# Performance work log

Measured on AMD Instinct MI355X. Metric: run time of the kernel, lower is better.

The kernel has to match this reference:

```python
import jax, jax.numpy as jnp
from jax import lax
import numpy as np

GAMMA = 1.0
BIG = 1e10  # stand-in for +inf; exp(-BIG/gamma) underflows to 0 and keeps grads finite


def pairwise_sq_euclidean(A, B):
    # A: (B,T1,K), B: (B,T2,K) -> (B,T1,T2); 0.5*||a-b||^2 expanded to avoid (B,T1,T2,K)
    aa = 0.5 * jnp.sum(A * A, axis=-1)  # (B,T1)
    bb = 0.5 * jnp.sum(B * B, axis=-1)  # (B,T2)
    ab = jnp.einsum('bik,bjk->bij', A, B)
    return aa[:, :, None] + bb[:, None, :] - ab


def soft_dtw(C, gamma):
    # C: (B, m, n). Sequential DP: V[i,j] = C[i-1,j-1] + softmin_gamma(V[i,j-1], V[i-1,j-1], V[i-1,j])
    Bsz, m, n = C.shape
    dt = C.dtype
    big = jnp.asarray(BIG, dt)
    # row 0 of V: V[0,0]=0, V[0,j]=inf
    v0 = jnp.concatenate([jnp.zeros((Bsz, 1), dt), jnp.full((Bsz, n), big, dt)], axis=1)

    def row_step(v_prev, c_row):
        # v_prev: (B, n+1) = V[i-1, :]; c_row: (B, n) = C[:, i-1, :]
        def col_step(v_left, inp):
            c, v_diag, v_up = inp  # each (B,)
            prev = jnp.stack([v_left, v_diag, v_up], axis=-1)  # (B,3)
            minv = -gamma * jax.nn.logsumexp(-prev / gamma, axis=-1)
            v_new = c + minv
            return v_new, v_new

        xs = (c_row.T, v_prev[:, :-1].T, v_prev[:, 1:].T)  # (n, B) each
        _, vals = lax.scan(col_step, jnp.full((Bsz,), big, dt), xs)
        v_row = jnp.concatenate([jnp.full((Bsz, 1), big, dt), vals.T], axis=1)
        return v_row, None

    v_final, _ = lax.scan(row_step, v0, jnp.moveaxis(C, 1, 0))
    return v_final[:, -1]  # (B,)


def setup_inputs() -> dict:
    key = jax.random.key(0)
    k1, k2 = jax.random.split(key)
    X = jax.random.normal(k1, (512, 256, 64), dtype=jnp.float32)
    Y = jax.random.normal(k2, (512, 256, 64), dtype=jnp.float32)
    return {"X": X, "Y": Y}


def reference(X, Y):
    gamma = jnp.asarray(GAMMA, X.dtype)
    s_xy = soft_dtw(pairwise_sq_euclidean(X, Y), gamma)
    s_xx = soft_dtw(pairwise_sq_euclidean(X, X), gamma)
    s_yy = soft_dtw(pairwise_sq_euclidean(Y, Y), gamma)
    D = s_xy - 0.5 * s_xx - 0.5 * s_yy
    # normalize=False, reduction='mean'
    return jnp.mean(D)
```

## Files before the change

kernel.cpp:

```cpp
#include <hip/hip_runtime.h>

typedef _Float16 h2 __attribute__((ext_vector_type(2)));
typedef _Float16 h8 __attribute__((ext_vector_type(8)));
typedef float f4 __attribute__((ext_vector_type(4)));

#define TT 256
#define KK 64
#define BIGV 1e10f
#define LOG2E 1.44269504f
#define LN2 0.69314718f
#define RL 32
#define RSTR 65

__device__ __forceinline__ float softmin3b(float a, float b, float c) {
  float m, d, M;
  asm("v_min3_f32 %0, %1, %2, %3" : "=v"(m) : "v"(a), "v"(b), "v"(c));
  asm("v_max3_f32 %0, %1, %2, %3" : "=v"(M) : "v"(a), "v"(b), "v"(c));
  asm("v_med3_f32 %0, %1, %2, %3" : "=v"(d) : "v"(a), "v"(b), "v"(c));
  float s = 1.0f + __builtin_amdgcn_exp2f(m - d) + __builtin_amdgcn_exp2f(m - M);
  return m - __log2f(s);
}

__global__ __launch_bounds__(64, 2)
void sdtw_fused1(const float* __restrict__ X, const float* __restrict__ Y,
                 float* __restrict__ out) {
  const int p = blockIdx.x;
  const int type = p >> 9;
  const int b = p & 511;
  const float* Ap = (type == 2 ? Y : X) + (size_t)b * TT * KK;
  const float* Bp = (type == 1 ? X : Y) + (size_t)b * TT * KK;
  const float wgt = (type == 0) ? (LN2 / 512.0f) : (-LN2 / 1024.0f);

  __shared__ unsigned int ring0[RL * RSTR];
  __shared__ unsigned int ring1[RL * RSTR];
  __shared__ float saa[TT];
  __shared__ float sbb[TT];

  const int t = threadIdx.x;
  const int hk = t >> 4, lr = t & 15;

  #pragma unroll
  for (int i = 0; i < 33; ++i) {
    int idx = i * 64 + t;
    if (idx < RL * RSTR) { ring0[idx] = 0u; ring1[idx] = 0u; }
  }

  h8 af[16][2];
  #pragma unroll
  for (int Rt = 0; Rt < 16; ++Rt) {
    float s = 0.f;
    #pragma unroll
    for (int kk = 0; kk < 2; ++kk) {
      const float4* src = (const float4*)(Ap + (Rt * 16 + lr) * KK + kk * 32 + hk * 8);
      float4 x = src[0], y = src[1];
      af[Rt][kk] = (h8){(_Float16)x.x, (_Float16)x.y, (_Float16)x.z, (_Float16)x.w,
                        (_Float16)y.x, (_Float16)y.y, (_Float16)y.z, (_Float16)y.w};
      s += x.x * x.x + x.y * x.y + x.z * x.z + x.w * x.w
         + y.x * y.x + y.y * y.y + y.z * y.z + y.w * y.w;
    }
    s += __shfl_xor(s, 16);
    s += __shfl_xor(s, 32);
    if (hk == (Rt & 3)) saa[Rt * 16 + lr] = 0.5f * LOG2E * s;
  }

  h8 bwin[4][2];
  float vL1 = BIGV, vL2 = BIGV, vL3 = BIGV, vL4 = BIGV;
  float dg = (t == 0) ? 0.0f : BIGV;

  #pragma unroll 1
  for (int kbo = 0; kbo < 5; ++kbo) {
    #pragma unroll
    for (int q = 0; q < 4; ++q) {
      const int KB = kbo * 4 + q;
      if (KB <= 15) {
        float s2 = 0.f;
        #pragma unroll
        for (int kk = 0; kk < 2; ++kk) {
          const float4* src = (const float4*)(Bp + (KB * 16 + lr) * KK + kk * 32 + hk * 8);
          float4 x = src[0], y = src[1];
          bwin[q][kk] = (h8){(_Float16)x.x, (_Float16)x.y, (_Float16)x.z, (_Float16)x.w,
                             (_Float16)y.x, (_Float16)y.y, (_Float16)y.z, (_Float16)y.w};
          s2 += x.x * x.x + x.y * x.y + x.z * x.z + x.w * x.w
              + y.x * y.x + y.y * y.y + y.z * y.z + y.w * y.w;
        }
        s2 += __shfl_xor(s2, 16);
        s2 += __shfl_xor(s2, 32);
        if (hk == 0) sbb[KB * 16 + lr] = 0.5f * LOG2E * s2;
      }
      if (KB <= 18) {
        #pragma unroll
        for (int r = 0; r < 4; ++r) {
          const int k = KB * 4 + r;
          #pragma unroll
          for (int dlt = 0; dlt < 4; ++dlt) {
            if (dlt <= KB && dlt >= KB - 15) {
              const int Rt = r + 4 * dlt;
              const int Ct = KB - dlt;
              const int slot = (q - dlt) & 3;
              f4 acc = {0.f, 0.f, 0.f, 0.f};
              acc = __builtin_amdgcn_mfma_f32_16x16x32_f16(af[Rt][0], bwin[slot][0], acc, 0, 0, 0);
              acc = __builtin_amdgcn_mfma_f32_16x16x32_f16(af[Rt][1], bwin[slot][1], acc, 0, 0, 0);
              const int r0 = Rt * 16 + hk * 4;
              f4 aav = *(const f4*)&saa[r0];
              float bbv = sbb[Ct * 16 + lr];
              float c0 = fmaf(-LOG2E, acc.x, aav.x + bbv);
              float c1 = fmaf(-LOG2E, acc.y, aav.y + bbv);
              float c2 = fmaf(-LOG2E, acc.z, aav.z + bbv);
              float c3 = fmaf(-LOG2E, acc.w, aav.w + bbv);
              const int t_row = 4 * Rt + hk;
              const int s1 = Ct * 16 + lr + t_row;
              const int widx = (s1 & 31) * RSTR + t_row;
              ring0[widx] = __builtin_bit_cast(unsigned int, __builtin_amdgcn_cvt_pkrtz(c0, c1));
              ring1[widx] = __builtin_bit_cast(unsigned int, __builtin_amdgcn_cvt_pkrtz(c2, c3));
            }
          }
          unsigned int w0[4], w1[4];
          #pragma unroll
          for (int u = 0; u < 4; ++u) {
            const int s1 = 4 * k + u;
            const int ridx = (s1 & 31) * RSTR + t;
            w0[u] = ring0[ridx];
            w1[u] = ring1[ridx];
          }
          #pragma unroll
          for (int u = 0; u < 4; ++u) {
            float up1 = __shfl_up(vL4, 1);
            if (t == 0) up1 = BIGV;
            h2 cA = __builtin_bit_cast(h2, w0[u]);
            h2 cB = __builtin_bit_cast(h2, w1[u]);
            float v1 = (float)cA[0] + softmin3b(vL1, dg, up1);
            float v2 = (float)cA[1] + softmin3b(vL2, vL1, v1);
            float v3 = (float)cB[0] + softmin3b(vL3, vL2, v2);
            float v4 = (float)cB[1] + softmin3b(vL4, vL3, v3);
            vL1 = v1; vL2 = v2; vL3 = v3; vL4 = v4; dg = up1;
          }
        }
      }
    }
  }

  #pragma unroll
  for (int u = 0; u < 15; ++u) {
    const int s1 = 304 + u;
    const int ridx = (s1 & 31) * RSTR + t;
    unsigned int a0 = ring0[ridx];
    unsigned int a1 = ring1[ridx];
    float up1 = __shfl_up(vL4, 1);
    if (t == 0) up1 = BIGV;
    h2 cA = __builtin_bit_cast(h2, a0);
    h2 cB = __builtin_bit_cast(h2, a1);
    float v1 = (float)cA[0] + softmin3b(vL1, dg, up1);
    float v2 = (float)cA[1] + softmin3b(vL2, vL1, v1);
    float v3 = (float)cB[0] + softmin3b(vL3, vL2, v2);
    float v4 = (float)cB[1] + softmin3b(vL4, vL3, v3);
    vL1 = v1; vL2 = v2; vL3 = v3; vL4 = v4; dg = up1;
  }

  if (t == 63) atomicAdd(out, wgt * vL4);
}

extern "C" void kernel_launch(void* const* d_in, const int* in_sizes, int n_in,
                              void* d_out, int out_size, void* d_ws, size_t ws_size,
                              hipStream_t stream) {
  const float* X = (const float*)d_in[0];
  const float* Y = (const float*)d_in[1];
  float* out = (float*)d_out;
  hipMemsetAsync(out, 0, sizeof(float) * out_size, stream);
  sdtw_fused1<<<1536, 64, 0, stream>>>(X, Y, out);
}
```

Baseline: 144.6 us.

## Split cost-matrix MFMA and DP recurrence into producer/consumer waves with fp8 inputs

Moves to two-wave blocks: wave 0 computes the pairwise cost tiles with MFMA and writes them to the LDS ring, and wave 1 runs the soft-DTW anti-diagonal recurrence one step behind, with a __syncthreads between steps. Inputs are quantized to fp8 and the fp8 MFMA is used, and the norms are taken from the quantized values, so the distance expansion stays consistent. The aim is to overlap matrix work with the serial softmin chain and to shorten MFMA and register cost. The trade-off is a block barrier every step and fp8 precision loss in the cost matrix, which could hurt accuracy.

```diff
diff --git a/kernel.cpp b/kernel.cpp
--- a/kernel.cpp
+++ b/kernel.cpp
@@ -1,7 +1,6 @@
 #include <hip/hip_runtime.h>
 
 typedef _Float16 h2 __attribute__((ext_vector_type(2)));
-typedef _Float16 h8 __attribute__((ext_vector_type(8)));
 typedef float f4 __attribute__((ext_vector_type(4)));
 
 #define TT 256
@@ -21,9 +20,17 @@
   return m - __log2f(s);
 }
 
-__global__ __launch_bounds__(64, 2)
-void sdtw_fused1(const float* __restrict__ X, const float* __restrict__ Y,
-                 float* __restrict__ out) {
+__device__ __forceinline__ float sumsq_fp8x4(unsigned int pk) {
+  float d0 = __builtin_amdgcn_cvt_f32_fp8((int)pk, 0);
+  float d1 = __builtin_amdgcn_cvt_f32_fp8((int)pk, 1);
+  float d2 = __builtin_amdgcn_cvt_f32_fp8((int)pk, 2);
+  float d3 = __builtin_amdgcn_cvt_f32_fp8((int)pk, 3);
+  return (d0 * d0 + d1 * d1) + (d2 * d2 + d3 * d3);
+}
+
+__global__ __launch_bounds__(128)
+void sdtw_pc(const float* __restrict__ X, const float* __restrict__ Y,
+             float* __restrict__ out) {
   const int p = blockIdx.x;
   const int type = p >> 9;
   const int b = p & 511;
@@ -34,129 +41,153 @@
   __shared__ unsigned int ring0[RL * RSTR];
   __shared__ unsigned int ring1[RL * RSTR];
   __shared__ float saa[TT];
-  __shared__ float sbb[TT];
-
-  const int t = threadIdx.x;
+
+  const int tid = threadIdx.x;
+  const int wv = tid >> 6;
+  const int t = tid & 63;
   const int hk = t >> 4, lr = t & 15;
 
   #pragma unroll
-  for (int i = 0; i < 33; ++i) {
-    int idx = i * 64 + t;
+  for (int i = 0; i < 17; ++i) {
+    int idx = i * 128 + tid;
     if (idx < RL * RSTR) { ring0[idx] = 0u; ring1[idx] = 0u; }
   }
 
-  h8 af[16][2];
-  #pragma unroll
-  for (int Rt = 0; Rt < 16; ++Rt) {
-    float s = 0.f;
+  uint2 af[16][2];
+  uint2 bwin[4][2];
+  float bbR[4];
+
+  if (wv == 0) {
     #pragma unroll
-    for (int kk = 0; kk < 2; ++kk) {
-      const float4* src = (const float4*)(Ap + (Rt * 16 + lr) * KK + kk * 32 + hk * 8);
-      float4 x = src[0], y = src[1];
-      af[Rt][kk] = (h8){(_Float16)x.x, (_Float16)x.y, (_Float16)x.z, (_Float16)x.w,
-                        (_Float16)y.x, (_Float16)y.y, (_Float16)y.z, (_Float16)y.w};
-      s += x.x * x.x + x.y * x.y + x.z * x.z + x.w * x.w
-         + y.x * y.x + y.y * y.y + y.z * y.z + y.w * y.w;
+    for (int Rt = 0; Rt < 16; ++Rt) {
+      float nrm = 0.f;
+      #pragma unroll
+      for (int kk = 0; kk < 2; ++kk) {
+        const float4* src = (const float4*)(Ap + (Rt * 16 + lr) * KK + kk * 32 + hk * 8);
+        float4 x = src[0], y = src[1];
+        unsigned int p0 = __builtin_amdgcn_cvt_pk_fp8_f32(x.x, x.y, 0, false);
+        p0 = __builtin_amdgcn_cvt_pk_fp8_f32(x.z, x.w, p0, true);
+        unsigned int p1 = __builtin_amdgcn_cvt_pk_fp8_f32(y.x, y.y, 0, false);
+        p1 = __builtin_amdgcn_cvt_pk_fp8_f32(y.z, y.w, p1, true);
+        af[Rt][kk] = make_uint2(p0, p1);
+        nrm += sumsq_fp8x4(p0) + sumsq_fp8x4(p1);
+      }
+      nrm += __shfl_xor(nrm, 16);
+      nrm += __shfl_xor(nrm, 32);
+      if (hk == 0) saa[Rt * 16 + lr] = 0.5f * LOG2E * nrm;
     }
-    s += __shfl_xor(s, 16);
-    s += __shfl_xor(s, 32);
-    if (hk == (Rt & 3)) saa[Rt * 16 + lr] = 0.5f * LOG2E * s;
-  }
-
-  h8 bwin[4][2];
+  }
+
   float vL1 = BIGV, vL2 = BIGV, vL3 = BIGV, vL4 = BIGV;
   float dg = (t == 0) ? 0.0f : BIGV;
+
+  __syncthreads();
 
   #pragma unroll 1
   for (int kbo = 0; kbo < 5; ++kbo) {
     #pragma unroll
     for (int q = 0; q < 4; ++q) {
       const int KB = kbo * 4 + q;
-      if (KB <= 15) {
-        float s2 = 0.f;
+      if (wv == 0 && KB <= 15) {
+        float nrm = 0.f;
         #pragma unroll
         for (int kk = 0; kk < 2; ++kk) {
           const float4* src = (const float4*)(Bp + (KB * 16 + lr) * KK + kk * 32 + hk * 8);
           float4 x = src[0], y = src[1];
-          bwin[q][kk] = (h8){(_Float16)x.x, (_Float16)x.y, (_Float16)x.z, (_Float16)x.w,
-                             (_Float16)y.x, (_Float16)y.y, (_Float16)y.z, (_Float16)y.w};
-          s2 += x.x * x.x + x.y * x.y + x.z * x.z + x.w * x.w
-              + y.x * y.x + y.y * y.y + y.z * y.z + y.w * y.w;
+          unsigned int p0 = __builtin_amdgcn_cvt_pk_fp8_f32(x.x, x.y, 0, false);
+          p0 = __builtin_amdgcn_cvt_pk_fp8_f32(x.z, x.w, p0, true);
+          unsigned int p1 = __builtin_amdgcn_cvt_pk_fp8_f32(y.x, y.y, 0, false);
+          p1 = __builtin_amdgcn_cvt_pk_fp8_f32(y.z, y.w, p1, true);
+          bwin[q][kk] = make_uint2(p0, p1);
+          nrm += sumsq_fp8x4(p0) + sumsq_fp8x4(p1);
         }
-        s2 += __shfl_xor(s2, 16);
-        s2 += __shfl_xor(s2, 32);
-        if (hk == 0) sbb[KB * 16 + lr] = 0.5f * LOG2E * s2;
+        nrm += __shfl_xor(nrm, 16);
+        nrm += __shfl_xor(nrm, 32);
+        bbR[q] = 0.5f * LOG2E * nrm;
       }
-      if (KB <= 18) {
-        #pragma unroll
-        for (int r = 0; r < 4; ++r) {
-          const int k = KB * 4 + r;
-          #pragma unroll
-          for (int dlt = 0; dlt < 4; ++dlt) {
-            if (dlt <= KB && dlt >= KB - 15) {
-              const int Rt = r + 4 * dlt;
-              const int Ct = KB - dlt;
-              const int slot = (q - dlt) & 3;
-              f4 acc = {0.f, 0.f, 0.f, 0.f};
-              acc = __builtin_amdgcn_mfma_f32_16x16x32_f16(af[Rt][0], bwin[slot][0], acc, 0, 0, 0);
-              acc = __builtin_amdgcn_mfma_f32_16x16x32_f16(af[Rt][1], bwin[slot][1], acc, 0, 0, 0);
-              const int r0 = Rt * 16 + hk * 4;
-              f4 aav = *(const f4*)&saa[r0];
-              float bbv = sbb[Ct * 16 + lr];
-              float c0 = fmaf(-LOG2E, acc.x, aav.x + bbv);
-              float c1 = fmaf(-LOG2E, acc.y, aav.y + bbv);
-              float c2 = fmaf(-LOG2E, acc.z, aav.z + bbv);
-              float c3 = fmaf(-LOG2E, acc.w, aav.w + bbv);
-              const int t_row = 4 * Rt + hk;
-              const int s1 = Ct * 16 + lr + t_row;
-              const int widx = (s1 & 31) * RSTR + t_row;
-              ring0[widx] = __builtin_bit_cast(unsigned int, __builtin_amdgcn_cvt_pkrtz(c0, c1));
-              ring1[widx] = __builtin_bit_cast(unsigned int, __builtin_amdgcn_cvt_pkrtz(c2, c3));
+      #pragma unroll
+      for (int r = 0; r < 4; ++r) {
+        const int k = KB * 4 + r;
+        if (wv == 0) {
+          if (KB <= 18) {
+            #pragma unroll
+            for (int dlt = 0; dlt < 4; ++dlt) {
+              if (dlt <= KB && KB - dlt <= 15) {
+                const int Rt = r + 4 * dlt;
+                const int slot = (q - dlt) & 3;
+                const int Ct = KB - dlt;
+                f4 acc = {0.f, 0.f, 0.f, 0.f};
+                acc = __builtin_amdgcn_mfma_f32_16x16x32_fp8_fp8(
+                        __builtin_bit_cast(long, af[Rt][0]),
+                        __builtin_bit_cast(long, bwin[slot][0]), acc, 0, 0, 0);
+                acc = __builtin_amdgcn_mfma_f32_16x16x32_fp8_fp8(
+                        __builtin_bit_cast(long, af[Rt][1]),
+                        __builtin_bit_cast(long, bwin[slot][1]), acc, 0, 0, 0);
+                f4 aav = *(const f4*)&saa[Rt * 16 + hk * 4];
+                float bbv = bbR[slot];
+                float c0 = fmaf(-LOG2E, acc.x, aav.x + bbv);
+                float c1 = fmaf(-LOG2E, acc.y, aav.y + bbv);
+                float c2 = fmaf(-LOG2E, acc.z, aav.z + bbv);
+                float c3 = fmaf(-LOG2E, acc.w, aav.w + bbv);
+                unsigned int pk01 = __builtin_bit_cast(unsigned int,
+                    __builtin_amdgcn_cvt_pkrtz(c0, c1));
+                unsigned int pk23 = __builtin_bit_cast(unsigned int,
+                    __builtin_amdgcn_cvt_pkrtz(c2, c3));
+                const int t_row = 4 * Rt + hk;
+                const int s1 = Ct * 16 + lr + t_row;
+                const int widx = (s1 & 31) * RSTR + t_row;
+                ring0[widx] = pk01;
+                ring1[widx] = pk23;
+              }
             }
           }
-          unsigned int w0[4], w1[4];
-          #pragma unroll
-          for (int u = 0; u < 4; ++u) {
-            const int s1 = 4 * k + u;
-            const int ridx = (s1 & 31) * RSTR + t;
-            w0[u] = ring0[ridx];
-            w1[u] = ring1[ridx];
-          }
-          #pragma unroll
-          for (int u = 0; u < 4; ++u) {
-            float up1 = __shfl_up(vL4, 1);
-            if (t == 0) up1 = BIGV;
-            h2 cA = __builtin_bit_cast(h2, w0[u]);
-            h2 cB = __builtin_bit_cast(h2, w1[u]);
-            float v1 = (float)cA[0] + softmin3b(vL1, dg, up1);
-            float v2 = (float)cA[1] + softmin3b(vL2, vL1, v1);
-            float v3 = (float)cB[0] + softmin3b(vL3, vL2, v2);
-            float v4 = (float)cB[1] + softmin3b(vL4, vL3, v3);
-            vL1 = v1; vL2 = v2; vL3 = v3; vL4 = v4; dg = up1;
+        } else {
+          const int kc = k - 1;
+          if (kc >= 0 && kc <= 75) {
+            unsigned int w0[4], w1[4];
+            #pragma unroll
+            for (int u = 0; u < 4; ++u) {
+              const int ridx = ((4 * kc + u) & 31) * RSTR + t;
+              w0[u] = ring0[ridx];
+              w1[u] = ring1[ridx];
+            }
+            #pragma unroll
+            for (int u = 0; u < 4; ++u) {
+              float up1 = __shfl_up(vL4, 1);
+              if (t == 0) up1 = BIGV;
+              h2 cA = __builtin_bit_cast(h2, w0[u]);
+              h2 cB = __builtin_bit_cast(h2, w1[u]);
+              float v1 = (float)cA[0] + softmin3b(vL1, dg, up1);
+              float v2 = (float)cA[1] + softmin3b(vL2, vL1, v1);
+              float v3 = (float)cB[0] + softmin3b(vL3, vL2, v2);
+              float v4 = (float)cB[1] + softmin3b(vL4, vL3, v3);
+              vL1 = v1; vL2 = v2; vL3 = v3; vL4 = v4; dg = up1;
+            }
           }
         }
+        __syncthreads();
       }
     }
   }
 
-  #pragma unroll
-  for (int u = 0; u < 15; ++u) {
-    const int s1 = 304 + u;
-    const int ridx = (s1 & 31) * RSTR + t;
-    unsigned int a0 = ring0[ridx];
-    unsigned int a1 = ring1[ridx];
-    float up1 = __shfl_up(vL4, 1);
-    if (t == 0) up1 = BIGV;
-    h2 cA = __builtin_bit_cast(h2, a0);
-    h2 cB = __builtin_bit_cast(h2, a1);
-    float v1 = (float)cA[0] + softmin3b(vL1, dg, up1);
-    float v2 = (float)cA[1] + softmin3b(vL2, vL1, v1);
-    float v3 = (float)cB[0] + softmin3b(vL3, vL2, v2);
-    float v4 = (float)cB[1] + softmin3b(vL4, vL3, v3);
-    vL1 = v1; vL2 = v2; vL3 = v3; vL4 = v4; dg = up1;
-  }
-
-  if (t == 63) atomicAdd(out, wgt * vL4);
+  if (wv == 1) {
+    #pragma unroll
+    for (int u = 0; u < 15; ++u) {
+      const int ridx = ((304 + u) & 31) * RSTR + t;
+      unsigned int a0 = ring0[ridx];
+      unsigned int a1 = ring1[ridx];
+      float up1 = __shfl_up(vL4, 1);
+      if (t == 0) up1 = BIGV;
+      h2 cA = __builtin_bit_cast(h2, a0);
+      h2 cB = __builtin_bit_cast(h2, a1);
+      float v1 = (float)cA[0] + softmin3b(vL1, dg, up1);
+      float v2 = (float)cA[1] + softmin3b(vL2, vL1, v1);
+      float v3 = (float)cB[0] + softmin3b(vL3, vL2, v2);
+      float v4 = (float)cB[1] + softmin3b(vL4, vL3, v3);
+      vL1 = v1; vL2 = v2; vL3 = v3; vL4 = v4; dg = up1;
+    }
+    if (t == 63) atomicAdd(out, wgt * vL4);
+  }
 }
 
 extern "C" void kernel_launch(void* const* d_in, const int* in_sizes, int n_in,
@@ -166,5 +197,5 @@
   const float* Y = (const float*)d_in[1];
   float* out = (float*)d_out;
   hipMemsetAsync(out, 0, sizeof(float) * out_size, stream);
-  sdtw_fused1<<<1536, 64, 0, stream>>>(X, Y, out);
-}
+  sdtw_pc<<<1536, 128, 0, stream>>>(X, Y, out);
+}
```

After: 178.2 us. 1.23x slower.
